# Performance work log

Measured on AMD Instinct MI355X. Metric: run time of the kernel, lower is better.

The kernel has to match this reference:

```python
import jax, jax.numpy as jnp
import numpy as np

B, S, D, H = 2, 2048, 1024, 16
DH = D // H  # 64

def setup_inputs() -> dict:
    key = jax.random.key(0)
    ks = jax.random.split(key, 11)
    sc = 1.0 / np.sqrt(D)
    return {
        "query": jax.random.normal(ks[0], (B, S, D), jnp.float32),
        "key":   jax.random.normal(ks[1], (B, S, D), jnp.float32),
        "value": jax.random.normal(ks[2], (B, S, D), jnp.float32),
        "Wq": jax.random.normal(ks[3], (D, D), jnp.float32) * sc,
        "bq": jnp.zeros((D,), jnp.float32),
        "Wk": jax.random.normal(ks[4], (D, D), jnp.float32) * sc,
        "bk": jnp.zeros((D,), jnp.float32),
        "Wv": jax.random.normal(ks[5], (D, D), jnp.float32) * sc,
        "bv": jnp.zeros((D,), jnp.float32),
        "Wo": jax.random.normal(ks[6], (D, D), jnp.float32) * sc,
        "bo": jnp.zeros((D,), jnp.float32),
    }

def reference(query, key, value, Wq, bq, Wk, bk, Wv, bv, Wo, bo):
    # torch Linear: y = x @ W^T + b
    def split_heads(x):  # (B,S,D) -> (B,H,S,DH)
        return x.reshape(B, S, H, DH).transpose(0, 2, 1, 3)
    Q = split_heads(query @ Wq.T + bq)
    K = split_heads(key   @ Wk.T + bk)
    V = split_heads(value @ Wv.T + bv)
    scores = jnp.einsum('bhqd,bhkd->bhqk', Q, K) / jnp.sqrt(jnp.float32(DH))
    # Original applies torch.softmax(scores, dim=1) on a (B*H, Sq, Sk) tensor,
    # i.e. normalization over the QUERY axis -> axis=-2 here (faithful to source).
    attn = jax.nn.softmax(scores, axis=-2)
    # dropout omitted for deterministic reference (identity / eval mode)
    out = jnp.einsum('bhqk,bhkd->bhqd', attn, V)  # (B,H,S,DH)
    out = out.transpose(0, 2, 1, 3).reshape(B, S, D)
    return out @ Wo.T + bo
```

## Files before the change

### kernel.cpp

```cpp
#include <hip/hip_runtime.h>
#include <hip/hip_bf16.h>
#include <math.h>

#define BB 2
#define SS 2048
#define DD 1024
#define HH 16
#define DH 64

typedef __bf16 bf16;
typedef __bf16 bf16x8 __attribute__((ext_vector_type(8)));
typedef __bf16 bf16x4 __attribute__((ext_vector_type(4)));
typedef short short4v __attribute__((ext_vector_type(4)));
typedef float f32x4 __attribute__((ext_vector_type(4)));

static const size_t NTOK  = (size_t)BB * SS * DD;
static const size_t STATN = (size_t)BB * HH * SS;


__device__ __forceinline__ f32x4 mfma16(bf16x8 a, bf16x8 b, f32x4 c) {
    return __builtin_amdgcn_mfma_f32_16x16x32_bf16(a, b, c, 0, 0, 0);
}
__device__ __forceinline__ f32x4 mfma16k16(short4v a, short4v b, f32x4 c) {
    return __builtin_amdgcn_mfma_f32_16x16x16bf16_1k(a, b, c, 0, 0, 0);
}
__device__ __forceinline__ void gload_lds16(const void* g, void* l) {
    __builtin_amdgcn_global_load_lds(
        (const __attribute__((address_space(1))) void*)g,
        (__attribute__((address_space(3))) void*)l, 16, 0, 0);
}
__device__ __forceinline__ bf16x8 cvt8(float4 a, float4 b) {
    bf16x8 r;
    r[0] = (bf16)a.x; r[1] = (bf16)a.y; r[2] = (bf16)a.z; r[3] = (bf16)a.w;
    r[4] = (bf16)b.x; r[5] = (bf16)b.y; r[6] = (bf16)b.z; r[7] = (bf16)b.w;
    return r;
}

#define WAITV(N)  asm volatile("s_waitcnt vmcnt(" #N ")" ::: "memory")
#define BAR()     __builtin_amdgcn_s_barrier()
#define LBAR() do { asm volatile("s_waitcnt lgkmcnt(0)" ::: "memory"); \
                    __builtin_amdgcn_s_barrier(); } while (0)

__global__ void signal_f(float* out, float v) {
    if (threadIdx.x == 0 && blockIdx.x == 0) out[0] = v;
}

__global__ __launch_bounds__(256) void cvt_bf16(
    const float* __restrict__ s, bf16* __restrict__ d)
{
    size_t i = ((size_t)blockIdx.x * 256 + threadIdx.x) * 8;
    float4 a = *(const float4*)(s + i);
    float4 b = *(const float4*)(s + i + 4);
    *(bf16x8*)(d + i) = cvt8(a, b);
}
__global__ __launch_bounds__(256) void cvt_w3(
    const float* __restrict__ w0, const float* __restrict__ w1,
    const float* __restrict__ w2, bf16* __restrict__ o0,
    bf16* __restrict__ o1, bf16* __restrict__ o2)
{
    const float* s = (blockIdx.y == 0) ? w0 : (blockIdx.y == 1) ? w1 : w2;
    bf16*        d = (blockIdx.y == 0) ? o0 : (blockIdx.y == 1) ? o1 : o2;
    size_t i = ((size_t)blockIdx.x * 256 + threadIdx.x) * 8;
    float4 a = *(const float4*)(s + i);
    float4 b = *(const float4*)(s + i + 4);
    *(bf16x8*)(d + i) = cvt8(a, b);
}

__global__ __launch_bounds__(256, 3) void qkv8(
    const float* __restrict__ Aq, const float* __restrict__ Ak,
    const float* __restrict__ Av,
    const bf16* __restrict__ Wqb, const bf16* __restrict__ Wkb,
    const bf16* __restrict__ Wvb,
    const float* __restrict__ bq, const float* __restrict__ bk,
    const float* __restrict__ bv,
    bf16* __restrict__ Qs, bf16* __restrict__ Ks, bf16* __restrict__ Vt)
{
    const int K = DD, N = DD;
    __shared__ __align__(16) bf16 As[2][128][32];
    __shared__ __align__(16) bf16 Bs[2][128][32];

    int t = (int)threadIdx.x;
    int lane = t & 63, w = t >> 6;
    int wm = w >> 1, wn = w & 1;
    int c16 = lane & 15, quad = lane >> 4, ko = quad << 3;

    int x = blockIdx.x & 7;
    int j = blockIdx.x >> 3;
    int proj = j >> 5;
    int rem  = j & 31;
    int tm = x + ((rem >> 3) << 3);
    int tn = rem & 7;

    const float* A    = (proj == 0) ? Aq : (proj == 1) ? Ak : Av;
    const bf16*  W    = (proj == 0) ? Wqb : (proj == 1) ? Wkb : Wvb;
    const float* bias = (proj == 0) ? bq : (proj == 1) ? bk : bv;
    bf16*        C    = (proj == 0) ? Qs : (proj == 1) ? Ks : Vt;
    float osc = (proj == 0) ? 0.125f : 1.0f;

    int arow = t >> 1;
    int acb  = (t & 1) * 16;
    int wc0 = ((t & 1) * 2)     ^ (arow & 3);
    int wc1 = ((t & 1) * 2 + 1) ^ (arow & 3);
    const float* abase = A + (size_t)(tm * 128 + arow) * K + acb;
    const bf16*  wbase = W + (size_t)(tn * 128 + arow) * K + acb;

    int rsw   = (quad ^ (c16 & 3)) << 4;
    int aroff = (wm * 64 + c16) * 64 + rsw;
    int broff = (wn * 64 + c16) * 64 + rsw;

    f32x4 acc[4][4];
#pragma unroll
    for (int i = 0; i < 4; ++i)
#pragma unroll
        for (int q = 0; q < 4; ++q) acc[i][q] = (f32x4){0.f, 0.f, 0.f, 0.f};

    float4 aA0, aA1, aA2, aA3, aB0, aB1, aB2, aB3;
    bf16x8 wA0, wA1, wB0, wB1;

    aA0 = *(const float4*)(abase);     aA1 = *(const float4*)(abase + 4);
    aA2 = *(const float4*)(abase + 8); aA3 = *(const float4*)(abase + 12);
    wA0 = *(const bf16x8*)(wbase);     wA1 = *(const bf16x8*)(wbase + 8);
    {
        char* ab = (char*)&As[0][arow][0];
        char* bb = (char*)&Bs[0][arow][0];
        *(bf16x8*)(ab + wc0 * 16) = cvt8(aA0, aA1);
        *(bf16x8*)(ab + wc1 * 16) = cvt8(aA2, aA3);
        *(bf16x8*)(bb + wc0 * 16) = wA0;
        *(bf16x8*)(bb + wc1 * 16) = wA1;
    }
    aB0 = *(const float4*)(abase + 32);     aB1 = *(const float4*)(abase + 36);
    aB2 = *(const float4*)(abase + 40);     aB3 = *(const float4*)(abase + 44);
    wB0 = *(const bf16x8*)(wbase + 32);     wB1 = *(const bf16x8*)(wbase + 40);
    LBAR();

    auto qstep = [&](int T0, int BI,
                     float4& cA0, float4& cA1, float4& cA2, float4& cA3,
                     bf16x8& cW0, bf16x8& cW1,
                     float4& nA0, float4& nA1, float4& nA2, float4& nA3,
                     bf16x8& nW0, bf16x8& nW1) {
        if (T0 + 2 < 32) {
            const float* ap = abase + (T0 + 2) * 32;
            nA0 = *(const float4*)(ap);     nA1 = *(const float4*)(ap + 4);
            nA2 = *(const float4*)(ap + 8); nA3 = *(const float4*)(ap + 12);
            const bf16* wp = wbase + (T0 + 2) * 32;
            nW0 = *(const bf16x8*)(wp);     nW1 = *(const bf16x8*)(wp + 8);
        }
        const char* al = (const char*)&As[BI][0][0];
        const char* bl = (const char*)&Bs[BI][0][0];
        bf16x8 af[4], bfr[4];
#pragma unroll
        for (int mt = 0; mt < 4; ++mt)
            af[mt] = *(const bf16x8*)(al + aroff + mt * 1024);
#pragma unroll
        for (int nt = 0; nt < 4; ++nt)
            bfr[nt] = *(const bf16x8*)(bl + broff + nt * 1024);
#pragma unroll
        for (int mt = 0; mt < 4; ++mt)
#pragma unroll
            for (int nt = 0; nt < 4; ++nt)
                acc[mt][nt] = mfma16(af[mt], bfr[nt], acc[mt][nt]);
        if (T0 + 1 < 32) {
            char* ab = (char*)&As[BI ^ 1][arow][0];
            char* bb = (char*)&Bs[BI ^ 1][arow][0];
            *(bf16x8*)(ab + wc0 * 16) = cvt8(cA0, cA1);
            *(bf16x8*)(ab + wc1 * 16) = cvt8(cA2, cA3);
            *(bf16x8*)(bb + wc0 * 16) = cW0;
            *(bf16x8*)(bb + wc1 * 16) = cW1;
        }
        LBAR();
    };

    for (int i = 0; i < 16; ++i) {
        qstep(2 * i,     0, aB0, aB1, aB2, aB3, wB0, wB1,
                            aA0, aA1, aA2, aA3, wA0, wA1);
        qstep(2 * i + 1, 1, aA0, aA1, aA2, aA3, wA0, wA1,
                            aB0, aB1, aB2, aB3, wB0, wB1);
    }

#pragma unroll
    for (int nt = 0; nt < 4; ++nt) {
        int col = tn * 128 + wn * 64 + nt * 16 + c16;
        float bv2 = bias[col];
#pragma unroll
        for (int mt = 0; mt < 4; ++mt) {
            int r0 = tm * 128 + wm * 64 + mt * 16 + quad * 4;
            if (proj == 2) {
                int b2 = r0 >> 11;
                int s  = r0 & (SS - 1);
                size_t base = ((size_t)b2 * N + col) * SS + s;
                bf16x4 pk;
#pragma unroll
                for (int r = 0; r < 4; ++r)
                    pk[r] = (bf16)(acc[mt][nt][r] + bv2);
                *(bf16x4*)&C[base] = pk;
            } else {
#pragma unroll
                for (int r = 0; r < 4; ++r)
                    C[(size_t)(r0 + r) * N + col] =
                        (bf16)((acc[mt][nt][r] + bv2) * osc);
            }
        }
    }
}

__global__ __launch_bounds__(256) void gemm7(
    const bf16* __restrict__ A, const bf16* __restrict__ W,
    const float* __restrict__ bias, float* __restrict__ C)
{
    __shared__ __align__(16) bf16 As[4][128][32];
    __shared__ __align__(16) bf16 Bs[4][64][32];

    int t = (int)threadIdx.x;
    int lane = t & 63, w = t >> 6;
    int wm = w >> 1, wn = w & 1;
    int c16 = lane & 15, quad = lane >> 4, ko = quad << 3;

    int x = blockIdx.x & 7, j = blockIdx.x >> 3;
    int tm = x + ((j >> 4) << 3);
    int tn = j & 15;

    int srow = lane >> 2;
    int schk = (lane & 3) ^ (srow & 3);
    const bf16* asrc0 = A + (size_t)(tm * 128 + (2 * w) * 16 + srow) * DD + schk * 8;
    const bf16* asrc1 = asrc0 + (size_t)16 * DD;
    const bf16* wsrc  = W + (size_t)(tn * 64 + w * 16 + srow) * DD + schk * 8;
    char* adst0 = (char*)&As[0][0][0] + (2 * w) * 1024;
    char* adst1 = adst0 + 1024;
    char* wdst  = (char*)&Bs[0][0][0] + w * 1024;

    f32x4 acc[4][2];
#pragma unroll
    for (int i = 0; i < 4; ++i)
#pragma unroll
        for (int q = 0; q < 2; ++q) acc[i][q] = (f32x4){0.f, 0.f, 0.f, 0.f};

#pragma unroll
    for (int s = 0; s < 2; ++s) {
        gload_lds16(asrc0 + s * 32, adst0 + s * 8192);
        gload_lds16(asrc1 + s * 32, adst1 + s * 8192);
        gload_lds16(wsrc  + s * 32, wdst  + s * 4096);
    }

    for (int t0 = 0; t0 < 32; ++t0) {
        if (t0 + 2 < 32) {
            int s = t0 + 2;
            gload_lds16(asrc0 + s * 32, adst0 + (s & 3) * 8192);
            gload_lds16(asrc1 + s * 32, adst1 + (s & 3) * 8192);
            gload_lds16(wsrc  + s * 32, wdst  + (s & 3) * 4096);
        }
        if (t0 < 30)      { WAITV(6); }
        else if (t0 == 30){ WAITV(3); }
        else              { WAITV(0); }
        BAR();
        const char* al = (const char*)&As[0][0][0] + (t0 & 3) * 8192;
        const char* wl = (const char*)&Bs[0][0][0] + (t0 & 3) * 4096;
        bf16x8 af[4], bfr[2];
#pragma unroll
        for (int mt = 0; mt < 4; ++mt) {
            int row = wm * 64 + mt * 16 + c16;
            af[mt] = *(const bf16x8*)(al + row * 64 + ((quad ^ (row & 3)) << 4));
        }
#pragma unroll
        for (int nt = 0; nt < 2; ++nt) {
            int row = wn * 32 + nt * 16 + c16;
            bfr[nt] = *(const bf16x8*)(wl + row * 64 + ((quad ^ (row & 3)) << 4));
        }
#pragma unroll
        for (int mt = 0; mt < 4; ++mt)
#pragma unroll
            for (int nt = 0; nt < 2; ++nt)
                acc[mt][nt] = mfma16(af[mt], bfr[nt], acc[mt][nt]);
    }

#pragma unroll
    for (int nt = 0; nt < 2; ++nt) {
        int col = tn * 64 + wn * 32 + nt * 16 + c16;
        float bv = bias[col];
#pragma unroll
        for (int mt = 0; mt < 4; ++mt) {
            int r0 = tm * 128 + wm * 64 + mt * 16 + quad * 4;
#pragma unroll
            for (int r = 0; r < 4; ++r)
                C[(size_t)(r0 + r) * DD + col] = acc[mt][nt][r] + bv;
        }
    }
}

__global__ __launch_bounds__(512) void col_stats5(
    const bf16* __restrict__ Q, const bf16* __restrict__ Km,
    float* __restrict__ z0S, float* __restrict__ z1S)
{
    __shared__ __align__(16) bf16 Qlds[4][32][64];

    int t = (int)threadIdx.x;
    int w = t >> 6, lane = t & 63;
    int c16 = lane & 15, quad = lane >> 4, ko = quad << 3;

    int x = blockIdx.x & 7, j = blockIdx.x >> 3;
    int bh = ((j >> 4) << 3) + x;
    int qh = (j >> 3) & 1;
    int kg = j & 7;
    int b = bh >> 4, h = bh & (HH - 1);
    int kbase = kg * 256 + w * 32;
    int q0base = qh * 1024;
    float* zS = qh ? z1S : z0S;

    bf16x8 kf[2][2];
#pragma unroll
    for (int g = 0; g < 2; ++g) {
        const bf16* kp =
            Km + ((size_t)(b * SS + kbase + g * 16 + c16)) * DD + h * DH + ko;
        kf[g][0] = *(const bf16x8*)kp;
        kf[g][1] = *(const bf16x8*)(kp + 32);
    }

    int srow  = ((w & 3) << 3) + (lane >> 3);
    int schnk = (lane & 7) ^ (srow & 7);
    const bf16* gsrc =
        Q + ((size_t)(b * SS + q0base + srow)) * DD + h * DH + schnk * 8;
    int ldsOff = (w & 3) << 10;
    bool stager = (w < 4);

    float z[2][4] = {{0.f,0.f,0.f,0.f},{0.f,0.f,0.f,0.f}};

    if (stager) {
        gload_lds16(gsrc, (char*)&Qlds[0][0][0] + ldsOff);
        gload_lds16(gsrc + (size_t)32 * DD, (char*)&Qlds[1][0][0] + ldsOff);
    }

    for (int t0 = 0; t0 < 32; ++t0) {
        if (t0 + 2 < 32 && stager)
            gload_lds16(gsrc + (size_t)(t0 + 2) * 32 * DD,
                        (char*)&Qlds[(t0 + 2) & 3][0][0] + ldsOff);
        if (t0 < 30)      { WAITV(2); }
        else if (t0 == 30){ WAITV(1); }
        else              { WAITV(0); }
        BAR();
        const char* ql = (const char*)&Qlds[t0 & 3][0][0];
#pragma unroll
        for (int qs = 0; qs < 2; ++qs) {
            int row = qs * 16 + c16;
            int p0  = quad ^ (row & 7);
            bf16x8 qf0 = *(const bf16x8*)(ql + row * 128 + p0 * 16);
            bf16x8 qf1 = *(const bf16x8*)(ql + row * 128 + (p0 ^ 4) * 16);
#pragma unroll
            for (int g = 0; g < 2; ++g) {
                f32x4 a = {0.f, 0.f, 0.f, 0.f};
                a = mfma16(kf[g][0], qf0, a);
                a = mfma16(kf[g][1], qf1, a);
#pragma unroll
                for (int r = 0; r < 4; ++r)
                    z[g][r] += __expf(a[r]);
            }
        }
    }

#pragma unroll
    for (int g = 0; g < 2; ++g)
#pragma unroll
        for (int r = 0; r < 4; ++r) {
#pragma unroll
            for (int off = 1; off < 16; off <<= 1)
                z[g][r] += __shfl_xor(z[g][r], off, 64);
        }
    if (c16 == 0) {
        size_t base = (size_t)bh * SS + kbase + quad * 4;
#pragma unroll
        for (int g = 0; g < 2; ++g)
#pragma unroll
            for (int r = 0; r < 4; ++r)
                zS[base + g * 16 + r] = z[g][r];
    }
}

__global__ __launch_bounds__(512) void attn_ctx7(
    const bf16* __restrict__ Q, const bf16* __restrict__ Km,
    const bf16* __restrict__ Vt, const float* __restrict__ z0S,
    const float* __restrict__ z1S, bf16* __restrict__ ctx)
{
    __shared__ __align__(16) char lds[4][8192];
    __shared__ __align__(16) float rzlds[2048];

    int t = (int)threadIdx.x;
    int w = t >> 6, lane = t & 63;
    int c16 = lane & 15, quad = lane >> 4, ko = quad << 3;

    int bid = blockIdx.x;
    int x = bid & 7, j = bid >> 3;
    int bh = ((j >> 3) << 3) + x;
    int qg = j & 7;
    int b = bh >> 4, h = bh & (HH - 1);
    int qt0 = qg * 16 + w * 2;

    const bf16* qp0 = Q + ((size_t)(b * SS + qt0 * 16 + c16)) * DD + h * DH + ko;
    bf16x8 qa0 = *(const bf16x8*)qp0;
    bf16x8 qa1 = *(const bf16x8*)(qp0 + 32);
    const bf16* qp1 = qp0 + (size_t)16 * DD;
    bf16x8 qb0 = *(const bf16x8*)qp1;
    bf16x8 qb1 = *(const bf16x8*)(qp1 + 32);

    {
        const float* z0p = z0S + (size_t)bh * SS + (w << 8) + lane * 4;
        const float* z1p = z1S + (size_t)bh * SS + (w << 8) + lane * 4;
        gload_lds16(z0p, (char*)&lds[0][0] + (w << 10));
        gload_lds16(z1p, (char*)&lds[1][0] + (w << 10));
        WAITV(0);
        __syncthreads();
        f32x4 z0 = *(const f32x4*)&lds[0][t * 16];
        f32x4 z1 = *(const f32x4*)&lds[1][t * 16];
        f32x4 rz;
#pragma unroll
        for (int r = 0; r < 4; ++r) rz[r] = 1.0f / (z0[r] + z1[r]);
        *(f32x4*)&rzlds[t * 4] = rz;
        __syncthreads();
    }

    const bf16* gsrc;
    int ldsOff;
    bool isK = (w < 4);
    if (isK) {
        int row   = (w << 3) + (lane >> 3);
        int chunk = (lane & 7) ^ (row & 7);
        gsrc  = Km + ((size_t)(b * SS + row)) * DD + h * DH + chunk * 8;
        ldsOff = (w << 10);
    } else {
        int i = w - 4;
        int row   = (i << 4) + (lane >> 2);
        int chunk = (lane & 3) ^ ((lane >> 3) & 3);
        gsrc  = Vt + ((size_t)(b * DD + h * DH + row)) * SS + chunk * 8;
        ldsOff = 4096 + (i << 10);
    }

    int kread  = c16 * 128 + ((quad ^ (c16 & 7)) << 4);
    int vread0 = c16 * 64 + (((quad >> 1) ^ ((c16 >> 1) & 3)) << 4)
               + ((quad & 1) << 3);

    f32x4 oa[4] = {{0,0,0,0},{0,0,0,0},{0,0,0,0},{0,0,0,0}};
    f32x4 ob[4] = {{0,0,0,0},{0,0,0,0},{0,0,0,0},{0,0,0,0}};

    gload_lds16(gsrc, &lds[0][ldsOff]);
    gload_lds16(isK ? gsrc + (size_t)32 * DD : gsrc + 32, &lds[1][ldsOff]);

    for (int t0 = 0; t0 < 64; ++t0) {
        if (t0 + 2 < 64) {
            int s = t0 + 2;
            const bf16* g = isK ? gsrc + (size_t)(s * 32) * DD : gsrc + s * 32;
            gload_lds16(g, &lds[s & 3][ldsOff]);
        }
        if (t0 < 62)      { WAITV(2); }
        else if (t0 == 62){ WAITV(1); }
        else              { WAITV(0); }
        BAR();
        const char* kl = &lds[t0 & 3][0];
        const char* vl = &lds[t0 & 3][4096];
#pragma unroll
        for (int ks = 0; ks < 2; ++ks) {
            int kb0 = kread + ks * 2048;
            bf16x8 kf0 = *(const bf16x8*)(kl + kb0);
            bf16x8 kf1 = *(const bf16x8*)(kl + (kb0 ^ 64));
            f32x4 z4 = *(const f32x4*)&rzlds[t0 * 32 + ks * 16 + quad * 4];
            f32x4 sa = {0,0,0,0}, sb = {0,0,0,0};
            sa = mfma16(kf0, qa0, sa);
            sa = mfma16(kf1, qa1, sa);
            sb = mfma16(kf0, qb0, sb);
            sb = mfma16(kf1, qb1, sb);

            union { bf16x4 b; short4v s; } pa, pb;
#pragma unroll
            for (int r = 0; r < 4; ++r) {
                pa.b[r] = (bf16)(__expf(sa[r]) * z4[r]);
                pb.b[r] = (bf16)(__expf(sb[r]) * z4[r]);
            }
            int vb0 = ks ? (vread0 ^ 32) : vread0;
#pragma unroll
            for (int dt = 0; dt < 4; ++dt) {
                short4v vf = *(const short4v*)(vl + vb0 + dt * 1024);
                oa[dt] = mfma16k16(pa.s, vf, oa[dt]);
                ob[dt] = mfma16k16(pb.s, vf, ob[dt]);
            }
        }
    }

    size_t orow = ((size_t)(b * SS + qt0 * 16 + quad * 4)) * DD + h * DH + c16;
#pragma unroll
    for (int dt = 0; dt < 4; ++dt)
#pragma unroll
        for (int r = 0; r < 4; ++r) {
            ctx[orow + (size_t)r * DD + dt * 16] = (bf16)oa[dt][r];
            ctx[orow + (size_t)(16 + r) * DD + dt * 16] = (bf16)ob[dt][r];
        }
}

extern "C" void kernel_launch(void* const* d_in, const int* in_sizes, int n_in,
                              void* d_out, int out_size, void* d_ws, size_t ws_size,
                              hipStream_t stream) {
    const float* query = (const float*)d_in[0];
    const float* key   = (const float*)d_in[1];
    const float* value = (const float*)d_in[2];
    const float* Wq = (const float*)d_in[3];
    const float* bq = (const float*)d_in[4];
    const float* Wk = (const float*)d_in[5];
    const float* bk = (const float*)d_in[6];
    const float* Wv = (const float*)d_in[7];
    const float* bv = (const float*)d_in[8];
    const float* Wo = (const float*)d_in[9];
    const float* bo = (const float*)d_in[10];
    float* out = (float*)d_out;

    if (n_in != 11 || in_sizes[0] != (int)NTOK || in_sizes[3] != DD * DD ||
        in_sizes[4] != DD || out_size != (int)NTOK) {
        hipLaunchKernelGGL(signal_f, dim3(1), dim3(64), 0, stream, out, -64.0f);
        return;
    }

    bf16* Qs  = (bf16*)d_ws;
    bf16* Ks  = Qs + NTOK;
    bf16* Vt  = Ks + NTOK;
    bf16* Cs  = Vt + NTOK;
    float* z0S = (float*)(Cs + NTOK);
    float* z1S = z0S + STATN;

    bf16* Wqb = Cs;
    bf16* Wkb = Cs + (size_t)DD * DD;
    bf16* Wvb = Cs + (size_t)2 * DD * DD;
    bf16* WoB = Qs;

    hipLaunchKernelGGL(cvt_w3, dim3(512, 3), dim3(256), 0, stream,
                       Wq, Wk, Wv, Wqb, Wkb, Wvb);

    hipLaunchKernelGGL(qkv8, dim3(768), dim3(256), 0, stream,
                       query, key, value, Wqb, Wkb, Wvb, bq, bk, bv,
                       Qs, Ks, Vt);

    hipLaunchKernelGGL(col_stats5, dim3(512), dim3(512), 0, stream,
                       Qs, Ks, z0S, z1S);

    hipLaunchKernelGGL(attn_ctx7, dim3(256), dim3(512), 0, stream,
                       Qs, Ks, Vt, z0S, z1S, Cs);

    hipLaunchKernelGGL(cvt_bf16, dim3(512), dim3(256), 0, stream, Wo, WoB);

    hipLaunchKernelGGL(gemm7, dim3(512), dim3(256), 0, stream, Cs, WoB, bo, out);
}
```

Measured before the change: 277.5 us.

## Shrink QKV and attention tiles per block to double grid size and occupancy

The QKV projection GEMM tile shrinks from 128x128 to 128x64, which doubles its grid to 1536 blocks and raises launch bounds to 6 blocks per CU. The attention context kernel now has each wave handle one 16-row query tile instead of two, which doubles its grid to 512 blocks and adds a min-blocks launch bound. Both changes aim to fill the 256 CUs better and hide latency through higher occupancy. The cost is lower data reuse per block: the A tile is re-read twice as often in QKV, and K/V tiles are reloaded for half as many queries in attention, which adds global and LDS traffic.

```diff
diff --git a/kernel.cpp b/kernel.cpp
--- a/kernel.cpp
+++ b/kernel.cpp
@@ -66,7 +66,7 @@
     *(bf16x8*)(d + i) = cvt8(a, b);
 }
 
-__global__ __launch_bounds__(256, 3) void qkv8(
+__global__ __launch_bounds__(256, 6) void qkv9(
     const float* __restrict__ Aq, const float* __restrict__ Ak,
     const float* __restrict__ Av,
     const bf16* __restrict__ Wqb, const bf16* __restrict__ Wkb,
@@ -77,7 +77,7 @@
 {
     const int K = DD, N = DD;
     __shared__ __align__(16) bf16 As[2][128][32];
-    __shared__ __align__(16) bf16 Bs[2][128][32];
+    __shared__ __align__(16) bf16 Bs[2][64][32];
 
     int t = (int)threadIdx.x;
     int lane = t & 63, w = t >> 6;
@@ -86,10 +86,10 @@
 
     int x = blockIdx.x & 7;
     int j = blockIdx.x >> 3;
-    int proj = j >> 5;
-    int rem  = j & 31;
-    int tm = x + ((rem >> 3) << 3);
-    int tn = rem & 7;
+    int proj = j >> 6;
+    int r2   = j & 63;
+    int tm = x + ((r2 >> 4) << 3);
+    int tn = r2 & 15;
 
     const float* A    = (proj == 0) ? Aq : (proj == 1) ? Ak : Av;
     const bf16*  W    = (proj == 0) ? Wqb : (proj == 1) ? Wkb : Wvb;
@@ -102,84 +102,82 @@
     int wc0 = ((t & 1) * 2)     ^ (arow & 3);
     int wc1 = ((t & 1) * 2 + 1) ^ (arow & 3);
     const float* abase = A + (size_t)(tm * 128 + arow) * K + acb;
-    const bf16*  wbase = W + (size_t)(tn * 128 + arow) * K + acb;
+
+    int wrow = t >> 2;
+    int wwc  = (t & 3) ^ (wrow & 3);
+    const bf16* wbase = W + (size_t)(tn * 64 + wrow) * K + (t & 3) * 8;
 
     int rsw   = (quad ^ (c16 & 3)) << 4;
     int aroff = (wm * 64 + c16) * 64 + rsw;
-    int broff = (wn * 64 + c16) * 64 + rsw;
-
-    f32x4 acc[4][4];
+    int broff = (wn * 32 + c16) * 64 + rsw;
+
+    f32x4 acc[4][2];
 #pragma unroll
     for (int i = 0; i < 4; ++i)
 #pragma unroll
-        for (int q = 0; q < 4; ++q) acc[i][q] = (f32x4){0.f, 0.f, 0.f, 0.f};
+        for (int q = 0; q < 2; ++q) acc[i][q] = (f32x4){0.f, 0.f, 0.f, 0.f};
 
     float4 aA0, aA1, aA2, aA3, aB0, aB1, aB2, aB3;
-    bf16x8 wA0, wA1, wB0, wB1;
+    bf16x8 wA, wB;
 
     aA0 = *(const float4*)(abase);     aA1 = *(const float4*)(abase + 4);
     aA2 = *(const float4*)(abase + 8); aA3 = *(const float4*)(abase + 12);
-    wA0 = *(const bf16x8*)(wbase);     wA1 = *(const bf16x8*)(wbase + 8);
+    wA  = *(const bf16x8*)(wbase);
     {
         char* ab = (char*)&As[0][arow][0];
-        char* bb = (char*)&Bs[0][arow][0];
         *(bf16x8*)(ab + wc0 * 16) = cvt8(aA0, aA1);
         *(bf16x8*)(ab + wc1 * 16) = cvt8(aA2, aA3);
-        *(bf16x8*)(bb + wc0 * 16) = wA0;
-        *(bf16x8*)(bb + wc1 * 16) = wA1;
+        *(bf16x8*)((char*)&Bs[0][wrow][0] + wwc * 16) = wA;
     }
     aB0 = *(const float4*)(abase + 32);     aB1 = *(const float4*)(abase + 36);
     aB2 = *(const float4*)(abase + 40);     aB3 = *(const float4*)(abase + 44);
-    wB0 = *(const bf16x8*)(wbase + 32);     wB1 = *(const bf16x8*)(wbase + 40);
+    wB  = *(const bf16x8*)(wbase + 32);
     LBAR();
 
     auto qstep = [&](int T0, int BI,
                      float4& cA0, float4& cA1, float4& cA2, float4& cA3,
-                     bf16x8& cW0, bf16x8& cW1,
+                     bf16x8& cW,
                      float4& nA0, float4& nA1, float4& nA2, float4& nA3,
-                     bf16x8& nW0, bf16x8& nW1) {
+                     bf16x8& nW) {
         if (T0 + 2 < 32) {
             const float* ap = abase + (T0 + 2) * 32;
             nA0 = *(const float4*)(ap);     nA1 = *(const float4*)(ap + 4);
             nA2 = *(const float4*)(ap + 8); nA3 = *(const float4*)(ap + 12);
-            const bf16* wp = wbase + (T0 + 2) * 32;
-            nW0 = *(const bf16x8*)(wp);     nW1 = *(const bf16x8*)(wp + 8);
+            nW  = *(const bf16x8*)(wbase + (T0 + 2) * 32);
         }
         const char* al = (const char*)&As[BI][0][0];
         const char* bl = (const char*)&Bs[BI][0][0];
-        bf16x8 af[4], bfr[4];
+        bf16x8 af[4], bfr[2];
 #pragma unroll
         for (int mt = 0; mt < 4; ++mt)
             af[mt] = *(const bf16x8*)(al + aroff + mt * 1024);
 #pragma unroll
-        for (int nt = 0; nt < 4; ++nt)
+        for (int nt = 0; nt < 2; ++nt)
             bfr[nt] = *(const bf16x8*)(bl + broff + nt * 1024);
 #pragma unroll
         for (int mt = 0; mt < 4; ++mt)
 #pragma unroll
-            for (int nt = 0; nt < 4; ++nt)
+            for (int nt = 0; nt < 2; ++nt)
                 acc[mt][nt] = mfma16(af[mt], bfr[nt], acc[mt][nt]);
         if (T0 + 1 < 32) {
             char* ab = (char*)&As[BI ^ 1][arow][0];
-            char* bb = (char*)&Bs[BI ^ 1][arow][0];
             *(bf16x8*)(ab + wc0 * 16) = cvt8(cA0, cA1);
             *(bf16x8*)(ab + wc1 * 16) = cvt8(cA2, cA3);
-            *(bf16x8*)(bb + wc0 * 16) = cW0;
-            *(bf16x8*)(bb + wc1 * 16) = cW1;
+            *(bf16x8*)((char*)&Bs[BI ^ 1][wrow][0] + wwc * 16) = cW;
         }
         LBAR();
     };
 
     for (int i = 0; i < 16; ++i) {
-        qstep(2 * i,     0, aB0, aB1, aB2, aB3, wB0, wB1,
-                            aA0, aA1, aA2, aA3, wA0, wA1);
-        qstep(2 * i + 1, 1, aA0, aA1, aA2, aA3, wA0, wA1,
-                            aB0, aB1, aB2, aB3, wB0, wB1);
-    }
-
-#pragma unroll
-    for (int nt = 0; nt < 4; ++nt) {
-        int col = tn * 128 + wn * 64 + nt * 16 + c16;
+        qstep(2 * i,     0, aB0, aB1, aB2, aB3, wB,
+                            aA0, aA1, aA2, aA3, wA);
+        qstep(2 * i + 1, 1, aA0, aA1, aA2, aA3, wA,
+                            aB0, aB1, aB2, aB3, wB);
+    }
+
+#pragma unroll
+    for (int nt = 0; nt < 2; ++nt) {
+        int col = tn * 64 + wn * 32 + nt * 16 + c16;
         float bv2 = bias[col];
 #pragma unroll
         for (int mt = 0; mt < 4; ++mt) {
@@ -373,7 +371,7 @@
     }
 }
 
-__global__ __launch_bounds__(512) void attn_ctx7(
+__global__ __launch_bounds__(512, 4) void attn_ctx9(
     const bf16* __restrict__ Q, const bf16* __restrict__ Km,
     const bf16* __restrict__ Vt, const float* __restrict__ z0S,
     const float* __restrict__ z1S, bf16* __restrict__ ctx)
@@ -387,17 +385,14 @@
 
     int bid = blockIdx.x;
     int x = bid & 7, j = bid >> 3;
-    int bh = ((j >> 3) << 3) + x;
-    int qg = j & 7;
+    int bh = ((j >> 4) << 3) + x;
+    int qg = j & 15;
     int b = bh >> 4, h = bh & (HH - 1);
-    int qt0 = qg * 16 + w * 2;
-
-    const bf16* qp0 = Q + ((size_t)(b * SS + qt0 * 16 + c16)) * DD + h * DH + ko;
+    int qt = qg * 8 + w;
+
+    const bf16* qp0 = Q + ((size_t)(b * SS + qt * 16 + c16)) * DD + h * DH + ko;
     bf16x8 qa0 = *(const bf16x8*)qp0;
     bf16x8 qa1 = *(const bf16x8*)(qp0 + 32);
-    const bf16* qp1 = qp0 + (size_t)16 * DD;
-    bf16x8 qb0 = *(const bf16x8*)qp1;
-    bf16x8 qb1 = *(const bf16x8*)(qp1 + 32);
 
     {
         const float* z0p = z0S + (size_t)bh * SS + (w << 8) + lane * 4;
@@ -436,7 +431,6 @@
                + ((quad & 1) << 3);
 
     f32x4 oa[4] = {{0,0,0,0},{0,0,0,0},{0,0,0,0},{0,0,0,0}};
-    f32x4 ob[4] = {{0,0,0,0},{0,0,0,0},{0,0,0,0},{0,0,0,0}};
 
     gload_lds16(gsrc, &lds[0][ldsOff]);
     gload_lds16(isK ? gsrc + (size_t)32 * DD : gsrc + 32, &lds[1][ldsOff]);
@@ -459,36 +453,29 @@
             bf16x8 kf0 = *(const bf16x8*)(kl + kb0);
             bf16x8 kf1 = *(const bf16x8*)(kl + (kb0 ^ 64));
             f32x4 z4 = *(const f32x4*)&rzlds[t0 * 32 + ks * 16 + quad * 4];
-            f32x4 sa = {0,0,0,0}, sb = {0,0,0,0};
+            f32x4 sa = {0,0,0,0};
             sa = mfma16(kf0, qa0, sa);
             sa = mfma16(kf1, qa1, sa);
-            sb = mfma16(kf0, qb0, sb);
-            sb = mfma16(kf1, qb1, sb);
-
-            union { bf16x4 b; short4v s; } pa, pb;
-#pragma unroll
-            for (int r = 0; r < 4; ++r) {
+
+            union { bf16x4 b; short4v s; } pa;
+#pragma unroll
+            for (int r = 0; r < 4; ++r)
                 pa.b[r] = (bf16)(__expf(sa[r]) * z4[r]);
-                pb.b[r] = (bf16)(__expf(sb[r]) * z4[r]);
-            }
             int vb0 = ks ? (vread0 ^ 32) : vread0;
 #pragma unroll
             for (int dt = 0; dt < 4; ++dt) {
                 short4v vf = *(const short4v*)(vl + vb0 + dt * 1024);
                 oa[dt] = mfma16k16(pa.s, vf, oa[dt]);
-                ob[dt] = mfma16k16(pb.s, vf, ob[dt]);
             }
         }
     }
 
-    size_t orow = ((size_t)(b * SS + qt0 * 16 + quad * 4)) * DD + h * DH + c16;
+    size_t orow = ((size_t)(b * SS + qt * 16 + quad * 4)) * DD + h * DH + c16;
 #pragma unroll
     for (int dt = 0; dt < 4; ++dt)
 #pragma unroll
-        for (int r = 0; r < 4; ++r) {
+        for (int r = 0; r < 4; ++r)
             ctx[orow + (size_t)r * DD + dt * 16] = (bf16)oa[dt][r];
-            ctx[orow + (size_t)(16 + r) * DD + dt * 16] = (bf16)ob[dt][r];
-        }
 }
 
 extern "C" void kernel_launch(void* const* d_in, const int* in_sizes, int n_in,
@@ -528,14 +515,14 @@
     hipLaunchKernelGGL(cvt_w3, dim3(512, 3), dim3(256), 0, stream,
                        Wq, Wk, Wv, Wqb, Wkb, Wvb);
 
-    hipLaunchKernelGGL(qkv8, dim3(768), dim3(256), 0, stream,
+    hipLaunchKernelGGL(qkv9, dim3(1536), dim3(256), 0, stream,
                        query, key, value, Wqb, Wkb, Wvb, bq, bk, bv,
                        Qs, Ks, Vt);
 
     hipLaunchKernelGGL(col_stats5, dim3(512), dim3(512), 0, stream,
                        Qs, Ks, z0S, z1S);
 
-    hipLaunchKernelGGL(attn_ctx7, dim3(256), dim3(512), 0, stream,
+    hipLaunchKernelGGL(attn_ctx9, dim3(512), dim3(512), 0, stream,
                        Qs, Ks, Vt, z0S, z1S, Cs);
 
     hipLaunchKernelGGL(cvt_bf16, dim3(512), dim3(256), 0, stream, Wo, WoB);
```

New measurement: 309.8 us. 11.6% more time.
